# Kernel optimization log

Measured on AMD Instinct MI355X. Metric: run time of the kernel, lower is better.

## Reference

```python
import jax, jax.numpy as jnp
import numpy as np

Q, B, D, NH, DH, DI, M = 1024, 4, 1024, 16, 64, 4096, 1024
K = Q + M  # klen
SCALE_W = 0.02
LN_EPS = 1e-5


def _layer_norm(x, g, b):
    mu = jnp.mean(x, axis=-1, keepdims=True)
    var = jnp.var(x, axis=-1, keepdims=True)
    return (x - mu) * jax.lax.rsqrt(var + LN_EPS) * g + b


def _rel_shift(x):
    # x: [qlen, klen, bsz, n_head] -> Transformer-XL relative shift
    q, k = x.shape[0], x.shape[1]
    zero_pad = jnp.zeros((q, 1) + x.shape[2:], x.dtype)
    x_padded = jnp.concatenate([zero_pad, x], axis=1)          # [q, k+1, b, n]
    x_padded = x_padded.reshape((k + 1, q) + x.shape[2:])      # [k+1, q, b, n]
    return x_padded[1:].reshape(x.shape)


def setup_inputs() -> dict:
    key = jax.random.key(0)
    ks = jax.random.split(key, 12)
    f32 = jnp.float32
    inp = {
        "w": jax.random.normal(ks[0], (Q, B, D), f32),
        "r": jax.random.normal(ks[1], (K, 1, D), f32),
        "mems": jax.random.normal(ks[2], (M, B, D), f32),
        "qkv_w": SCALE_W * jax.random.normal(ks[3], (D, 3 * NH * DH), f32),
        "r_net_w": SCALE_W * jax.random.normal(ks[4], (D, NH * DH), f32),
        "o_w": SCALE_W * jax.random.normal(ks[5], (NH * DH, D), f32),
        "r_w_bias": SCALE_W * jax.random.normal(ks[6], (NH, DH), f32),
        "r_r_bias": SCALE_W * jax.random.normal(ks[7], (NH, DH), f32),
        "ln1_g": jnp.ones((D,), f32),
        "ln1_b": jnp.zeros((D,), f32),
        "ff_w1": SCALE_W * jax.random.normal(ks[8], (D, DI), f32),
        "ff_b1": jnp.zeros((DI,), f32),
        "ff_w2": SCALE_W * jax.random.normal(ks[9], (DI, D), f32),
        "ff_b2": jnp.zeros((D,), f32),
        "ln2_g": jnp.ones((D,), f32),
        "ln2_b": jnp.zeros((D,), f32),
        # causal mask with memory: query i attends to keys j <= i + mem_len
        "attn_mask": jnp.arange(K)[None, :] > (jnp.arange(Q)[:, None] + M),
    }
    return inp


def reference(w, r, mems, qkv_w, r_net_w, o_w, r_w_bias, r_r_bias,
              ln1_g, ln1_b, ff_w1, ff_b1, ff_w2, ff_b2, ln2_g, ln2_b,
              attn_mask):
    qlen, bsz = w.shape[0], w.shape[1]
    # --- relative multi-head attention (post-lnorm, mems concat) ---
    cat = jnp.concatenate([mems, w], axis=0)                   # [klen, b, d]
    w_heads = cat @ qkv_w                                      # [klen, b, 3*nh*dh]
    r_head_k = (r @ r_net_w).reshape(-1, NH, DH)               # [rlen, nh, dh]
    q_h, k_h, v_h = jnp.split(w_heads, 3, axis=-1)
    klen = k_h.shape[0]
    q_h = q_h[-qlen:].reshape(qlen, bsz, NH, DH)
    k_h = k_h.reshape(klen, bsz, NH, DH)
    v_h = v_h.reshape(klen, bsz, NH, DH)

    rw_q = q_h + r_w_bias[None, None]                          # [q, b, nh, dh]
    AC = jnp.einsum('ibnd,jbnd->ijbn', rw_q, k_h)
    rr_q = q_h + r_r_bias[None, None]
    BD = jnp.einsum('ibnd,jnd->ijbn', rr_q, r_head_k)
    BD = _rel_shift(BD)

    scale = 1.0 / (DH ** 0.5)
    attn_score = (AC + BD) * scale                             # [q, k, b, nh]
    attn_score = jnp.where(attn_mask[:, :, None, None], -jnp.inf, attn_score)
    attn_prob = jax.nn.softmax(attn_score, axis=1)
    attn_vec = jnp.einsum('ijbn,jbnd->ibnd', attn_prob, v_h)
    attn_out = attn_vec.reshape(qlen, bsz, NH * DH) @ o_w      # [q, b, d]
    out = _layer_norm(w + attn_out, ln1_g, ln1_b)

    # --- position-wise FFN (post-lnorm) ---
    core = jax.nn.relu(out @ ff_w1 + ff_b1) @ ff_w2 + ff_b2
    out = _layer_norm(out + core, ln2_g, ln2_b)
    return out
```

## Files before the change

### kernel.cpp

```cpp
#include <hip/hip_runtime.h>
#include <math.h>


#define QLEN 1024
#define BSZ  4
#define DMODEL 1024
#define NHEAD 16
#define DHEAD 64
#define DINNER 4096
#define MEMLEN 1024
#define KLEN 2048

typedef __attribute__((ext_vector_type(8))) short short8;
typedef __attribute__((ext_vector_type(4))) short short4_t;
typedef __attribute__((ext_vector_type(4))) float f32x4;

__device__ __forceinline__ unsigned short f2bf(float x) {
  union { float f; unsigned u; } cv; cv.f = x;
  const unsigned u = cv.u;
  return (unsigned short)((u + 0x7FFFu + ((u >> 16) & 1u)) >> 16);
}
__device__ __forceinline__ float bf2f(unsigned short b) {
  union { unsigned u; float f; } cv; cv.u = ((unsigned)b) << 16;
  return cv.f;
}

__device__ __forceinline__ void gload16(const void* g, void* l) {
  __builtin_amdgcn_global_load_lds(
      (const __attribute__((address_space(1))) unsigned int*)g,
      (__attribute__((address_space(3))) unsigned int*)l, 16, 0, 0);
}

__device__ __forceinline__ int chidx(int row, int kc) {
  return row * 4 + (kc ^ ((row >> 1) & 3));
}

template<int MODE>
__global__ __launch_bounds__(512) void mgemm2(
    const unsigned short* __restrict__ A, const unsigned short* __restrict__ Bt,
    unsigned short* __restrict__ Cb, const float* __restrict__ aux,
    unsigned short* __restrict__ oK, unsigned short* __restrict__ oV,
    int Kdim, int N)
{
  __shared__ __align__(16) char smem[98304];

  const int tid = threadIdx.x;
  const int lane = tid & 63, wv = tid >> 6;
  const int wr = wv >> 2, wc = wv & 3;
  const int quad = lane >> 4, l15 = lane & 15;

  const int gx = (int)gridDim.x;
  const int nwg = gx * (int)gridDim.y;
  const int flat = (int)blockIdx.y * gx + (int)blockIdx.x;
  const int swz = (flat & 7) * (nwg >> 3) + (flat >> 3);
  const int m0 = (swz / gx) * 256, n0 = (swz % gx) * 256;

  const int srow = tid >> 2;
  const int skc = (tid & 3) ^ ((srow >> 1) & 3);
  const unsigned short* pA0 = A + (size_t)(m0 + srow) * Kdim + skc * 8;
  const unsigned short* pA1 = A + (size_t)(m0 + 128 + srow) * Kdim + skc * 8;
  const unsigned short* pB0 = Bt + (size_t)(n0 + srow) * Kdim + skc * 8;
  const unsigned short* pB1 = Bt + (size_t)(n0 + 128 + srow) * Kdim + skc * 8;
  const int wb = (tid & 448) * 16;

  const int cch = (quad ^ ((l15 >> 1) & 3)) * 16;
  const int aoffb = wr * 8192 + l15 * 64 + cch;
  const int boffb = (wc >> 1) * 8192 + ((wc & 1) * 64 + l15) * 64 + cch;

  f32x4 acc[8][4] = {};

  const int nkt = Kdim >> 5;
  gload16(pA0, smem + wb);
  gload16(pA1, smem + 8192 + wb);
  gload16(pB0, smem + 49152 + wb);
  gload16(pB1, smem + 57344 + wb);
  pA0 += 32; pA1 += 32; pB0 += 32; pB1 += 32;
  gload16(pA0, smem + 16384 + wb);
  gload16(pA1, smem + 24576 + wb);
  gload16(pB0, smem + 65536 + wb);
  gload16(pB1, smem + 73728 + wb);
  pA0 += 32; pA1 += 32; pB0 += 32; pB1 += 32;

  int rbuf = 0;
  for (int kt = 0; kt < nkt; ++kt) {
    if (kt + 2 < nkt) {
      int wb3 = rbuf + 2; if (wb3 >= 3) wb3 -= 3;
      const int ab = wb3 * 16384, bb = 49152 + wb3 * 16384;
      gload16(pA0, smem + ab + wb);
      gload16(pA1, smem + ab + 8192 + wb);
      gload16(pB0, smem + bb + wb);
      gload16(pB1, smem + bb + 8192 + wb);
      pA0 += 32; pA1 += 32; pB0 += 32; pB1 += 32;
      asm volatile("s_waitcnt vmcnt(8)" ::: "memory");
    } else if (kt + 1 < nkt) {
      asm volatile("s_waitcnt vmcnt(4)" ::: "memory");
    } else {
      asm volatile("s_waitcnt vmcnt(0)" ::: "memory");
    }
    __builtin_amdgcn_s_barrier();

    const char* const abuf = smem + rbuf * 16384;
    const char* const bbuf = smem + 49152 + rbuf * 16384;

    short8 bfr[4], af[4];
#pragma unroll
    for (int j = 0; j < 4; ++j)
      bfr[j] = *(const short8*)(bbuf + boffb + j * 1024);
#pragma unroll
    for (int i = 0; i < 4; ++i)
      af[i] = *(const short8*)(abuf + aoffb + i * 1024);
    __builtin_amdgcn_s_setprio(1);
#pragma unroll
    for (int i = 0; i < 4; ++i)
#pragma unroll
      for (int j = 0; j < 4; ++j)
        acc[i][j] = __builtin_amdgcn_mfma_f32_16x16x32_bf16(
            af[i], bfr[j], acc[i][j], 0, 0, 0);
    __builtin_amdgcn_s_setprio(0);
    __builtin_amdgcn_s_barrier();

#pragma unroll
    for (int i = 0; i < 4; ++i)
      af[i] = *(const short8*)(abuf + aoffb + (i + 4) * 1024);
    __builtin_amdgcn_s_setprio(1);
#pragma unroll
    for (int i = 0; i < 4; ++i)
#pragma unroll
      for (int j = 0; j < 4; ++j)
        acc[i + 4][j] = __builtin_amdgcn_mfma_f32_16x16x32_bf16(
            af[i], bfr[j], acc[i + 4][j], 0, 0, 0);
    __builtin_amdgcn_s_setprio(0);
    asm volatile("s_waitcnt lgkmcnt(0)" ::: "memory");
    __builtin_amdgcn_s_barrier();
    rbuf += 1; if (rbuf == 3) rbuf = 0;
  }

  const int rb0 = m0 + wr * 128 + quad * 4;
  const int cb0 = n0 + wc * 64 + l15;
#pragma unroll
  for (int i = 0; i < 8; ++i) {
#pragma unroll
    for (int r = 0; r < 4; ++r) {
      const int grow = rb0 + i * 16 + r;
#pragma unroll
      for (int j = 0; j < 4; ++j) {
        const int gcol = cb0 + j * 16;
        const float v = acc[i][j][r];
        if constexpr (MODE == 0) {
          const int kkg = grow >> 2, b2 = grow & 3;
          const int sec = gcol >> 10, hn = (gcol >> 6) & 15, d = gcol & 63;
          const unsigned short bv = f2bf(v);
          if (sec == 0) {
            if (kkg >= MEMLEN)
              Cb[((size_t)(b2 * NHEAD + hn) * QLEN + (kkg - MEMLEN)) * DHEAD + d] = bv;
          } else if (sec == 1) {
            oK[((size_t)(b2 * NHEAD + hn) * KLEN + kkg) * DHEAD + d] = bv;
          } else {
            oV[((size_t)(b2 * NHEAD + hn) * KLEN + kkg) * DHEAD + d] = bv;
          }
        } else {
          Cb[(size_t)grow * N + gcol] = f2bf(fmaxf(v + aux[gcol], 0.f));
        }
      }
    }
  }
}

template<int MODE, int TN>
__global__ __launch_bounds__(256) void mgemm(
    const unsigned short* __restrict__ A, const unsigned short* __restrict__ Bt,
    float* __restrict__ C, unsigned short* __restrict__ Cb,
    const float* __restrict__ aux, const float* __restrict__ res,
    int Kdim, int N)
{
  constexpr int BUF = 8192 + TN * 64;
  __shared__ __align__(16) char smem[3 * BUF];

  const int tid = threadIdx.x;
  const int lane = tid & 63, wv = tid >> 6;

  const int gx = (int)gridDim.x;
  const int nwg = gx * (int)gridDim.y;
  const int flat = (int)blockIdx.y * gx + (int)blockIdx.x;
  const int swz = (flat & 7) * (nwg >> 3) + (flat >> 3);
  const int m0 = (swz / gx) * 128, n0 = (swz % gx) * TN;

  const unsigned short *gA0, *gA1, *gB0;
  {
    int c = tid, m = c >> 2, kc = (c & 3) ^ ((m >> 1) & 3);
    gA0 = A + (size_t)(m0 + m) * Kdim + kc * 8;
    c = 256 + tid; m = c >> 2; kc = (c & 3) ^ ((m >> 1) & 3);
    gA1 = A + (size_t)(m0 + m) * Kdim + kc * 8;
    c = tid; int nn = c >> 2; kc = (c & 3) ^ ((nn >> 1) & 3);
    gB0 = Bt + (size_t)(n0 + nn) * Kdim + kc * 8;
  }
  const int wvoff = (tid & 192) * 16;

  const int fr = lane & 15, kq = lane >> 4;
  constexpr int NJ = TN / 32;
  int aoff[4], boff[NJ];
#pragma unroll
  for (int t = 0; t < 4; ++t) {
    const int ra = (wv & 1) * 64 + t * 16 + fr;
    aoff[t] = chidx(ra, kq) * 16;
  }
#pragma unroll
  for (int t = 0; t < NJ; ++t) {
    const int rb = (wv >> 1) * (TN / 2) + t * 16 + fr;
    boff[t] = 8192 + chidx(rb, kq) * 16;
  }

  f32x4 acc[4][NJ] = {};

  {
    char* const b0 = smem + wvoff;
    gload16(gA0, b0);
    gload16(gA1, b0 + 4096);
    gload16(gB0, b0 + 8192);
    gA0 += 32; gA1 += 32; gB0 += 32;
    char* const b1 = smem + BUF + wvoff;
    gload16(gA0, b1);
    gload16(gA1, b1 + 4096);
    gload16(gB0, b1 + 8192);
    gA0 += 32; gA1 += 32; gB0 += 32;
  }

  int rbuf = 0;
  for (int k0 = 0; k0 < Kdim; k0 += 32) {
    if (k0 + 64 < Kdim) {
      int wb3 = rbuf + 2; if (wb3 >= 3) wb3 -= 3;
      char* const nb = smem + wb3 * BUF + wvoff;
      gload16(gA0, nb);
      gload16(gA1, nb + 4096);
      gload16(gB0, nb + 8192);
      gA0 += 32; gA1 += 32; gB0 += 32;
      asm volatile("s_waitcnt vmcnt(6)" ::: "memory");
    } else if (k0 + 32 < Kdim) {
      asm volatile("s_waitcnt vmcnt(3)" ::: "memory");
    } else {
      asm volatile("s_waitcnt vmcnt(0)" ::: "memory");
    }
    __builtin_amdgcn_s_barrier();

    const char* const cb = smem + rbuf * BUF;
    short8 af[4], bfr[NJ];
#pragma unroll
    for (int t = 0; t < 4; ++t) af[t] = *(const short8*)(cb + aoff[t]);
#pragma unroll
    for (int t = 0; t < NJ; ++t) bfr[t] = *(const short8*)(cb + boff[t]);
#pragma unroll
    for (int i = 0; i < 4; ++i)
#pragma unroll
      for (int j = 0; j < NJ; ++j)
        acc[i][j] = __builtin_amdgcn_mfma_f32_16x16x32_bf16(
            af[i], bfr[j], acc[i][j], 0, 0, 0);

    asm volatile("s_waitcnt lgkmcnt(0)" ::: "memory");
    __builtin_amdgcn_s_barrier();
    rbuf += 1; if (rbuf == 3) rbuf = 0;
  }

  const int rbase = m0 + (wv & 1) * 64 + (lane >> 4) * 4;
  const int cbase = n0 + (wv >> 1) * (TN / 2) + (lane & 15);
#pragma unroll
  for (int i = 0; i < 4; ++i) {
#pragma unroll
    for (int r = 0; r < 4; ++r) {
      const int grow = rbase + i * 16 + r;
#pragma unroll
      for (int j = 0; j < NJ; ++j) {
        const int gcol = cbase + j * 16;
        const float v = acc[i][j][r];
        if constexpr (MODE == 1) {
          const int hn = gcol >> 6, d = gcol & 63;
          Cb[((size_t)hn * KLEN + grow) * DHEAD + d] = f2bf(v);
        } else if constexpr (MODE == 2) {
          C[(size_t)grow * N + gcol] = v + res[(size_t)grow * N + gcol];
        } else {
          C[(size_t)grow * N + gcol] = v + aux[gcol] + res[(size_t)grow * N + gcol];
        }
      }
    }
  }
}

__global__ __launch_bounds__(256) void transpose_v(
    const unsigned short* __restrict__ Vh, unsigned short* __restrict__ Vt)
{
  __shared__ unsigned short t[64 * 80];
  const int j0 = (int)blockIdx.x * 64;
  const int bn = (int)blockIdx.y;
  const int tid = threadIdx.x;
#pragma unroll
  for (int it = 0; it < 2; ++it) {
    const int f = it * 256 + tid;
    const int j = f >> 3, d8 = (f & 7) * 8;
    const short8 v = *(const short8*)(Vh + ((size_t)bn * KLEN + j0 + j) * DHEAD + d8);
    *(short8*)(t + j * 80 + d8) = v;
  }
  __syncthreads();
  const int d = tid >> 2, jseg = (tid & 3) * 16;
  short8 o0, o1;
#pragma unroll
  for (int e = 0; e < 8; ++e) o0[e] = (short)t[(jseg + e) * 80 + d];
#pragma unroll
  for (int e = 0; e < 8; ++e) o1[e] = (short)t[(jseg + 8 + e) * 80 + d];
  unsigned short* op = Vt + ((size_t)bn * DHEAD + d) * KLEN + j0 + jseg;
  *(short8*)op = o0;
  *(short8*)(op + 8) = o1;
}

__global__ __launch_bounds__(256) void cast_all(
    const float* __restrict__ mems, const float* __restrict__ w,
    const float* __restrict__ r, unsigned short* __restrict__ Xcat,
    unsigned short* __restrict__ Rb16)
{
  const size_t i = ((size_t)blockIdx.x * 256 + threadIdx.x) * 8;
  const float* src;
  unsigned short* dst;
  if (i < 4194304)       { src = mems + i;          dst = Xcat + i; }
  else if (i < 8388608)  { src = w + (i - 4194304); dst = Xcat + i; }
  else                   { src = r + (i - 8388608); dst = Rb16 + (i - 8388608); }
  const float4 x = *(const float4*)src;
  const float4 y = *(const float4*)(src + 4);
  short8 v;
  v[0] = (short)f2bf(x.x); v[1] = (short)f2bf(x.y);
  v[2] = (short)f2bf(x.z); v[3] = (short)f2bf(x.w);
  v[4] = (short)f2bf(y.x); v[5] = (short)f2bf(y.y);
  v[6] = (short)f2bf(y.z); v[7] = (short)f2bf(y.w);
  *(short8*)dst = v;
}

__global__ __launch_bounds__(256) void transpose_all(
    const float* __restrict__ qkv_w, const float* __restrict__ r_net_w,
    const float* __restrict__ o_w, const float* __restrict__ ff_w1,
    const float* __restrict__ ff_w2,
    unsigned short* __restrict__ Wqkv, unsigned short* __restrict__ Wr,
    unsigned short* __restrict__ Wo, unsigned short* __restrict__ W1,
    unsigned short* __restrict__ W2)
{
  const int bid = (int)blockIdx.x;
  const float* in; unsigned short* out; int R, C, xt, loc;
  if (bid < 768)        { in = qkv_w;   out = Wqkv; R = 1024; C = 3072; xt = 48; loc = bid; }
  else if (bid < 1024)  { in = r_net_w; out = Wr;   R = 1024; C = 1024; xt = 16; loc = bid - 768; }
  else if (bid < 1280)  { in = o_w;     out = Wo;   R = 1024; C = 1024; xt = 16; loc = bid - 1024; }
  else if (bid < 2304)  { in = ff_w1;   out = W1;   R = 1024; C = 4096; xt = 64; loc = bid - 1280; }
  else                  { in = ff_w2;   out = W2;   R = 4096; C = 1024; xt = 16; loc = bid - 2304; }
  const int c0 = (loc % xt) * 64, r0 = (loc / xt) * 64;

  __shared__ float t[64][65];
  const int tid = threadIdx.x;
  const int rr = tid >> 4, cc = (tid & 15) * 4;
#pragma unroll
  for (int it = 0; it < 4; ++it) {
    const int rw = rr + it * 16;
    const float4 v = *(const float4*)(in + (size_t)(r0 + rw) * C + c0 + cc);
    t[rw][cc] = v.x; t[rw][cc + 1] = v.y; t[rw][cc + 2] = v.z; t[rw][cc + 3] = v.w;
  }
  __syncthreads();
  const int oc = tid >> 2, ob = (tid & 3) * 16;
#pragma unroll
  for (int j4 = 0; j4 < 4; ++j4) {
    short4_t o;
#pragma unroll
    for (int j = 0; j < 4; ++j) o[j] = (short)f2bf(t[ob + j4 * 4 + j][oc]);
    *(short4_t*)(out + (size_t)(c0 + oc) * R + r0 + ob + j4 * 4) = o;
  }
}

__global__ __launch_bounds__(256, 2) void attn_mfma(
    const unsigned short* __restrict__ Qh, const unsigned short* __restrict__ Kh,
    const unsigned short* __restrict__ Vt, const unsigned short* __restrict__ Rk,
    const float* __restrict__ rwb, const float* __restrict__ rrb,
    float* __restrict__ Opart0, float* __restrict__ Opart1,
    float* __restrict__ den0, float* __restrict__ den1)
{
  __shared__ __align__(16) char smem[65536];

  const int tid = threadIdx.x;
  const int lane = tid & 63, wv = tid >> 6;
  const int quad = lane >> 4, l15 = lane & 15;

  const int bid0 = (int)blockIdx.y * 32 + (int)blockIdx.x;
  const int slot = bid0 >> 3;
  const int bn = (bid0 & 7) * 8 + (slot >> 5);
  const int inner = slot & 31;
  const int it = inner >> 1, sp = inner & 1;
  const int i0 = it * 64;
  const int n = bn & 15;

  const int nch = 17 + it;
  const int h = (nch + 1) >> 1;
  const int lo = sp ? h : 0, hi = sp ? nch : h;

  const unsigned short* __restrict__ Qb = Qh + (size_t)bn * QLEN * DHEAD;
  const unsigned short* __restrict__ Kb = Kh + (size_t)bn * KLEN * DHEAD;
  const unsigned short* __restrict__ Vb = Vt + (size_t)bn * DHEAD * KLEN;
  const unsigned short* __restrict__ Rb = Rk + (size_t)n * KLEN * DHEAD;

  short8 qk[2], qr[2];
  {
    const int qrow = i0 + wv * 16 + l15;
    const unsigned short* qp = Qb + (size_t)qrow * DHEAD + quad * 8;
    const float* wp = rwb + n * DHEAD + quad * 8;
    const float* rp = rrb + n * DHEAD + quad * 8;
#pragma unroll
    for (int ks = 0; ks < 2; ++ks) {
      const short8 q8 = *(const short8*)(qp + ks * 32);
#pragma unroll
      for (int e = 0; e < 8; ++e) {
        const float qv = bf2f((unsigned short)q8[e]);
        qk[ks][e] = (short)f2bf(qv + wp[ks * 32 + e]);
        qr[ks][e] = (short)f2bf(qv + rp[ks * 32 + e]);
      }
    }
  }

  int srcl[4];
  bool condE[4];
#pragma unroll
  for (int r = 0; r < 4; ++r) {
    const int E = l15 - quad * 4 - r + 15;
    srcl[r] = (lane & 48) | (E & 15);
    condE[r] = (E >= 16);
  }

  f32x4 O[4] = {};
  float rden[4] = {0.f, 0.f, 0.f, 0.f};
  const int wvoff = (tid & 192) * 16;

  {
    const int j0 = lo * 64;
    const int g64 = lo - it + 15;
    const int rb3 = (g64 % 3) * 64;
#pragma unroll
    for (int t2 = 0; t2 < 2; ++t2) {
      const int s = t2 * 256 + tid;
      const int row = s >> 3, kc = (s & 7) ^ (row & 7);
      gload16(Kb + (((size_t)(j0 + row)) << 6) + kc * 8,
              smem + t2 * 4096 + wvoff);
    }
#pragma unroll
    for (int t2 = 0; t2 < 2; ++t2) {
      const int s = t2 * 256 + tid;
      const int row = s >> 3, kc = (s & 7) ^ (row & 7);
      gload16(Vb + (((size_t)row) << 11) + j0 + kc * 8,
              smem + 16384 + t2 * 4096 + wvoff);
    }
    const int gw = j0 - i0 + 960;
#pragma unroll
    for (int t2 = 0; t2 < 4; ++t2) {
      const int rr = t2 * 32 + (tid >> 3);
      const int gr = gw + rr;
      const int kc = (tid & 7) ^ (rr & 7);
      int pb = rb3 + t2 * 32; if (pb >= 192) pb -= 192;
      gload16(Rb + (((size_t)gr) << 6) + kc * 8,
              smem + 32768 + pb * 128 + wvoff);
    }
  }

  int cur = 0;
  for (int ch = lo; ch < hi; ++ch) {
    const int j0 = ch * 64;
    const int g64 = ch - it + 15;
    const int rb3 = (g64 % 3) * 64;
    const int gw = j0 - i0 + 960;

    asm volatile("s_waitcnt lgkmcnt(0)" ::: "memory");
    __builtin_amdgcn_s_barrier();

    if (ch + 1 < hi) {
      const int nb = cur ^ 1;
      const int j0n = j0 + 64;
#pragma unroll
      for (int t2 = 0; t2 < 2; ++t2) {
        const int s = t2 * 256 + tid;
        const int row = s >> 3, kc = (s & 7) ^ (row & 7);
        gload16(Kb + (((size_t)(j0n + row)) << 6) + kc * 8,
                smem + nb * 8192 + t2 * 4096 + wvoff);
      }
#pragma unroll
      for (int t2 = 0; t2 < 2; ++t2) {
        const int s = t2 * 256 + tid;
        const int row = s >> 3, kc = (s & 7) ^ (row & 7);
        gload16(Vb + (((size_t)row) << 11) + j0n + kc * 8,
                smem + 16384 + nb * 8192 + t2 * 4096 + wvoff);
      }
#pragma unroll
      for (int t2 = 0; t2 < 2; ++t2) {
        const int rr = t2 * 32 + (tid >> 3);
        const int gr = gw + 128 + rr;
        const int kc = (tid & 7) ^ (rr & 7);
        int pb = rb3 + 128 + t2 * 32; if (pb >= 192) pb -= 192;
        gload16(Rb + (((size_t)gr) << 6) + kc * 8,
                smem + 32768 + pb * 128 + wvoff);
      }
      asm volatile("s_waitcnt vmcnt(6)" ::: "memory");
    } else {
      asm volatile("s_waitcnt vmcnt(0)" ::: "memory");
    }
    __builtin_amdgcn_s_barrier();

    const char* const kbase = smem + cur * 8192;
    const char* const vbase = smem + 16384 + cur * 8192;

    f32x4 sk[4];
#pragma unroll
    for (int jt = 0; jt < 4; ++jt) {
      f32x4 a = {0.f, 0.f, 0.f, 0.f};
#pragma unroll
      for (int ks = 0; ks < 2; ++ks) {
        const int frr = jt * 16 + l15;
        const int c = (ks * 4 + quad) ^ (l15 & 7);
        const short8 kf = *(const short8*)(kbase + (frr * 8 + c) * 16);
        a = __builtin_amdgcn_mfma_f32_16x16x32_bf16(qk[ks], kf, a, 0, 0, 0);
      }
      sk[jt] = a;
    }
    f32x4 uu[5];
#pragma unroll
    for (int s = 0; s < 5; ++s) {
      f32x4 a = {0.f, 0.f, 0.f, 0.f};
      int frr = rb3 + (3 - wv + s) * 16 + l15;
      if (frr >= 192) frr -= 192;
#pragma unroll
      for (int ks = 0; ks < 2; ++ks) {
        const int c = (ks * 4 + quad) ^ (l15 & 7);
        const short8 rf = *(const short8*)(smem + 32768 + (frr * 8 + c) * 16);
        a = __builtin_amdgcn_mfma_f32_16x16x32_bf16(qr[ks], rf, a, 0, 0, 0);
      }
      uu[s] = a;
    }

    float rot[5][4];
#pragma unroll
    for (int s = 0; s < 5; ++s)
#pragma unroll
      for (int r = 0; r < 4; ++r)
        rot[s][r] = __shfl(uu[s][r], srcl[r], 64);

    unsigned short* const Ps = (unsigned short*)(smem + 57344);
#pragma unroll
    for (int jt = 0; jt < 4; ++jt) {
      const int jl = jt * 16 + l15;
#pragma unroll
      for (int r = 0; r < 4; ++r) {
        const int il = wv * 16 + quad * 4 + r;
        const int dj = (j0 + jl) - (i0 + il);
        const float uv = condE[r] ? rot[jt + 1][r] : rot[jt][r];
        const float sv = (sk[jt][r] + uv) * 0.125f;
        const float p = (dj <= 1024) ? __expf(sv) : 0.f;
        rden[r] += p;
        Ps[(il * 8 + ((jl >> 3) ^ (il & 7))) * 8 + (jl & 7)] = f2bf(p);
      }
    }

#pragma unroll
    for (int ks = 0; ks < 2; ++ks) {
      const int frp = wv * 16 + l15;
      const int cp = (ks * 4 + quad) ^ (l15 & 7);
      const short8 pf = *(const short8*)(smem + 57344 + (frp * 8 + cp) * 16);
#pragma unroll
      for (int dt = 0; dt < 4; ++dt) {
        const int vr = dt * 16 + l15;
        const short8 vf = *(const short8*)(vbase + (vr * 8 + cp) * 16);
        O[dt] = __builtin_amdgcn_mfma_f32_16x16x32_bf16(pf, vf, O[dt], 0, 0, 0);
      }
    }
    cur ^= 1;
  }

#pragma unroll
  for (int m = 1; m < 16; m <<= 1)
#pragma unroll
    for (int r = 0; r < 4; ++r)
      rden[r] += __shfl_xor(rden[r], m, 64);

  float* const Op = sp ? Opart1 : Opart0;
  float* const dp = sp ? den1 : den0;
  const size_t ob = (size_t)(bn * 16 + it) * 64;
#pragma unroll
  for (int r = 0; r < 4; ++r) {
    const int il = wv * 16 + quad * 4 + r;
#pragma unroll
    for (int dt = 0; dt < 4; ++dt)
      Op[(ob + il) * 64 + dt * 16 + l15] = O[dt][r];
    if (l15 == 0) dp[ob + il] = rden[r];
  }
}

__global__ __launch_bounds__(256) void attn_combine(
    const float* __restrict__ O0, const float* __restrict__ O1,
    const float* __restrict__ d0, const float* __restrict__ d1,
    unsigned short* __restrict__ AVb)
{
  const int blk = (int)blockIdx.x;
  const int bn = blk >> 4, it = blk & 15;
  const int b = bn >> 4, n = bn & 15;
  const int tid = threadIdx.x;
  const int il = tid >> 2, ds = (tid & 3) * 16;
  const size_t base = ((size_t)blk * 64 + il) * 64 + ds;
  const float inv = 1.f / (d0[blk * 64 + il] + d1[blk * 64 + il]);
  short8 o0, o1;
#pragma unroll
  for (int g = 0; g < 2; ++g) {
    const float4 a = *(const float4*)(O0 + base + g * 8);
    const float4 bb = *(const float4*)(O1 + base + g * 8);
    const float4 a2 = *(const float4*)(O0 + base + g * 8 + 4);
    const float4 b2 = *(const float4*)(O1 + base + g * 8 + 4);
    short8& o = g ? o1 : o0;
    o[0] = (short)f2bf((a.x + bb.x) * inv);  o[1] = (short)f2bf((a.y + bb.y) * inv);
    o[2] = (short)f2bf((a.z + bb.z) * inv);  o[3] = (short)f2bf((a.w + bb.w) * inv);
    o[4] = (short)f2bf((a2.x + b2.x) * inv); o[5] = (short)f2bf((a2.y + b2.y) * inv);
    o[6] = (short)f2bf((a2.z + b2.z) * inv); o[7] = (short)f2bf((a2.w + b2.w) * inv);
  }
  unsigned short* op =
      AVb + ((size_t)(it * 64 + il) * BSZ + b) * DMODEL + n * DHEAD + ds;
  *(short8*)op = o0;
  *(short8*)(op + 8) = o1;
}

__global__ __launch_bounds__(256) void ln_kernel(
    float* __restrict__ X, const float* __restrict__ gw,
    const float* __restrict__ bw, unsigned short* __restrict__ bfo)
{
  const int row = blockIdx.x, tid = threadIdx.x;
  float* rp = X + (size_t)row * DMODEL;
  const float4 x = *(const float4*)(rp + tid * 4);
  float s = x.x + x.y + x.z + x.w;
  float q = x.x * x.x + x.y * x.y + x.z * x.z + x.w * x.w;
#pragma unroll
  for (int m = 1; m < 64; m <<= 1) {
    s += __shfl_xor(s, m, 64);
    q += __shfl_xor(q, m, 64);
  }
  __shared__ float ss[4], sq[4];
  if ((tid & 63) == 0) { ss[tid >> 6] = s; sq[tid >> 6] = q; }
  __syncthreads();
  s = ss[0] + ss[1] + ss[2] + ss[3];
  q = sq[0] + sq[1] + sq[2] + sq[3];
  const float mu = s * (1.f / DMODEL);
  const float var = q * (1.f / DMODEL) - mu * mu;
  const float rstd = rsqrtf(var + 1e-5f);
  const float4 g4 = *(const float4*)(gw + tid * 4);
  const float4 b4 = *(const float4*)(bw + tid * 4);
  float4 y;
  y.x = (x.x - mu) * rstd * g4.x + b4.x;
  y.y = (x.y - mu) * rstd * g4.y + b4.y;
  y.z = (x.z - mu) * rstd * g4.z + b4.z;
  y.w = (x.w - mu) * rstd * g4.w + b4.w;
  *(float4*)(rp + tid * 4) = y;
  if (bfo) {
    short4_t o;
    o[0] = (short)f2bf(y.x); o[1] = (short)f2bf(y.y);
    o[2] = (short)f2bf(y.z); o[3] = (short)f2bf(y.w);
    *(short4_t*)(bfo + (size_t)row * DMODEL + tid * 4) = o;
  }
}

extern "C" void kernel_launch(void* const* d_in, const int* in_sizes, int n_in,
                              void* d_out, int out_size, void* d_ws,
                              size_t ws_size, hipStream_t stream)
{
  const float* w       = (const float*)d_in[0];
  const float* r       = (const float*)d_in[1];
  const float* mems    = (const float*)d_in[2];
  const float* qkv_w   = (const float*)d_in[3];
  const float* r_net_w = (const float*)d_in[4];
  const float* o_w     = (const float*)d_in[5];
  const float* r_w_bias= (const float*)d_in[6];
  const float* r_r_bias= (const float*)d_in[7];
  const float* ln1_g   = (const float*)d_in[8];
  const float* ln1_b   = (const float*)d_in[9];
  const float* ff_w1   = (const float*)d_in[10];
  const float* ff_b1   = (const float*)d_in[11];
  const float* ff_w2   = (const float*)d_in[12];
  const float* ff_b2   = (const float*)d_in[13];
  const float* ln2_g   = (const float*)d_in[14];
  const float* ln2_b   = (const float*)d_in[15];
  float* out = (float*)d_out;

  float* X1 = (float*)d_ws;
  unsigned short* Qh   = (unsigned short*)(X1 + 4194304);
  unsigned short* Kh   = Qh + 4194304;
  unsigned short* Vt   = Kh + 8388608;
  unsigned short* Rk   = Vt + 8388608;
  unsigned short* Xcat = Rk + 2097152 + 8192;
  unsigned short* Wqkv = Xcat + 8388608;
  unsigned short* Wr   = Wqkv + 3145728;
  unsigned short* Wo   = Wr + 1048576;
  unsigned short* W1   = Wo + 1048576;
  unsigned short* W2   = W1 + 4194304;
  float* den0 = (float*)(W2 + 4194304);
  float* den1 = den0 + 65536;
  unsigned short* AVb  = (unsigned short*)(den1 + 65536);
  unsigned short* Vh     = (unsigned short*)X1;
  unsigned short* Rb16   = AVb;
  float* Opart0          = (float*)X1;
  float* Opart1          = (float*)Xcat;
  unsigned short* X1b    = Qh;
  unsigned short* H      = Kh;

  const dim3 blk(256);
  const dim3 blk2(512);

  cast_all<<<dim3(5120), blk, 0, stream>>>(mems, w, r, Xcat, Rb16);
  transpose_all<<<dim3(3328), blk, 0, stream>>>(
      qkv_w, r_net_w, o_w, ff_w1, ff_w2, Wqkv, Wr, Wo, W1, W2);

  mgemm2<0><<<dim3(12, 32), blk2, 0, stream>>>(
      Xcat, Wqkv, Qh, nullptr, Kh, Vh, DMODEL, 3 * DMODEL);
  transpose_v<<<dim3(32, 64), blk, 0, stream>>>(Vh, Vt);
  mgemm<1, 64><<<dim3(16, 16), blk, 0, stream>>>(
      Rb16, Wr, nullptr, Rk, nullptr, nullptr, DMODEL, DMODEL);
  attn_mfma<<<dim3(32, 64), blk, 0, stream>>>(
      Qh, Kh, Vt, Rk, r_w_bias, r_r_bias, Opart0, Opart1, den0, den1);
  attn_combine<<<dim3(1024), blk, 0, stream>>>(Opart0, Opart1, den0, den1, AVb);
  mgemm<2, 64><<<dim3(16, 32), blk, 0, stream>>>(
      AVb, Wo, X1, nullptr, nullptr, w, DMODEL, DMODEL);
  ln_kernel<<<dim3(4096), blk, 0, stream>>>(X1, ln1_g, ln1_b, X1b);
  mgemm2<3><<<dim3(16, 16), blk2, 0, stream>>>(
      X1b, W1, H, ff_b1, nullptr, nullptr, DMODEL, DINNER);
  mgemm<4, 64><<<dim3(16, 32), blk, 0, stream>>>(
      H, W2, out, nullptr, ff_b2, X1, DINNER, DMODEL);
  ln_kernel<<<dim3(4096), blk, 0, stream>>>(out, ln2_g, ln2_b, nullptr);

  (void)in_sizes; (void)n_in; (void)out_size; (void)ws_size;
}
```

Baseline: 521.2 us.

## Load R fragments directly from global to shrink LDS and raise occupancy

The attention kernel no longer stages the relative-position R tile in a rotating shared-memory ring buffer. Each wave now loads its R fragments straight from global memory into registers every chunk. This cuts shared memory from 64KB to 40KB, and the launch bound is raised to allow 3 blocks per CU. The cost is uncoalesced, unprefetched global loads on the critical path each iteration, plus more register pressure under a tighter register budget.

```diff
diff --git a/kernel.cpp b/kernel.cpp
--- a/kernel.cpp
+++ b/kernel.cpp
@@ -368,14 +368,14 @@
   }
 }
 
-__global__ __launch_bounds__(256, 2) void attn_mfma(
+__global__ __launch_bounds__(256, 3) void attn_mfma(
     const unsigned short* __restrict__ Qh, const unsigned short* __restrict__ Kh,
     const unsigned short* __restrict__ Vt, const unsigned short* __restrict__ Rk,
     const float* __restrict__ rwb, const float* __restrict__ rrb,
     float* __restrict__ Opart0, float* __restrict__ Opart1,
     float* __restrict__ den0, float* __restrict__ den1)
 {
-  __shared__ __align__(16) char smem[65536];
+  __shared__ __align__(16) char smem[40960];
 
   const int tid = threadIdx.x;
   const int lane = tid & 63, wv = tid >> 6;
@@ -431,8 +431,6 @@
 
   {
     const int j0 = lo * 64;
-    const int g64 = lo - it + 15;
-    const int rb3 = (g64 % 3) * 64;
 #pragma unroll
     for (int t2 = 0; t2 < 2; ++t2) {
       const int s = t2 * 256 + tid;
@@ -447,23 +445,11 @@
       gload16(Vb + (((size_t)row) << 11) + j0 + kc * 8,
               smem + 16384 + t2 * 4096 + wvoff);
     }
-    const int gw = j0 - i0 + 960;
-#pragma unroll
-    for (int t2 = 0; t2 < 4; ++t2) {
-      const int rr = t2 * 32 + (tid >> 3);
-      const int gr = gw + rr;
-      const int kc = (tid & 7) ^ (rr & 7);
-      int pb = rb3 + t2 * 32; if (pb >= 192) pb -= 192;
-      gload16(Rb + (((size_t)gr) << 6) + kc * 8,
-              smem + 32768 + pb * 128 + wvoff);
-    }
   }
 
   int cur = 0;
   for (int ch = lo; ch < hi; ++ch) {
     const int j0 = ch * 64;
-    const int g64 = ch - it + 15;
-    const int rb3 = (g64 % 3) * 64;
     const int gw = j0 - i0 + 960;
 
     asm volatile("s_waitcnt lgkmcnt(0)" ::: "memory");
@@ -486,20 +472,20 @@
         gload16(Vb + (((size_t)row) << 11) + j0n + kc * 8,
                 smem + 16384 + nb * 8192 + t2 * 4096 + wvoff);
       }
-#pragma unroll
-      for (int t2 = 0; t2 < 2; ++t2) {
-        const int rr = t2 * 32 + (tid >> 3);
-        const int gr = gw + 128 + rr;
-        const int kc = (tid & 7) ^ (rr & 7);
-        int pb = rb3 + 128 + t2 * 32; if (pb >= 192) pb -= 192;
-        gload16(Rb + (((size_t)gr) << 6) + kc * 8,
-                smem + 32768 + pb * 128 + wvoff);
-      }
-      asm volatile("s_waitcnt vmcnt(6)" ::: "memory");
+      asm volatile("s_waitcnt vmcnt(4)" ::: "memory");
     } else {
       asm volatile("s_waitcnt vmcnt(0)" ::: "memory");
     }
     __builtin_amdgcn_s_barrier();
+
+    short8 rfr0[5], rfr1[5];
+#pragma unroll
+    for (int s = 0; s < 5; ++s) {
+      const int gr = gw + (3 - wv + s) * 16 + l15;
+      const unsigned short* rp = Rb + (((size_t)gr) << 6) + quad * 8;
+      rfr0[s] = *(const short8*)rp;
+      rfr1[s] = *(const short8*)(rp + 32);
+    }
 
     const char* const kbase = smem + cur * 8192;
     const char* const vbase = smem + 16384 + cur * 8192;
@@ -521,14 +507,8 @@
 #pragma unroll
     for (int s = 0; s < 5; ++s) {
       f32x4 a = {0.f, 0.f, 0.f, 0.f};
-      int frr = rb3 + (3 - wv + s) * 16 + l15;
-      if (frr >= 192) frr -= 192;
-#pragma unroll
-      for (int ks = 0; ks < 2; ++ks) {
-        const int c = (ks * 4 + quad) ^ (l15 & 7);
-        const short8 rf = *(const short8*)(smem + 32768 + (frr * 8 + c) * 16);
-        a = __builtin_amdgcn_mfma_f32_16x16x32_bf16(qr[ks], rf, a, 0, 0, 0);
-      }
+      a = __builtin_amdgcn_mfma_f32_16x16x32_bf16(qr[0], rfr0[s], a, 0, 0, 0);
+      a = __builtin_amdgcn_mfma_f32_16x16x32_bf16(qr[1], rfr1[s], a, 0, 0, 0);
       uu[s] = a;
     }
 
@@ -539,7 +519,7 @@
       for (int r = 0; r < 4; ++r)
         rot[s][r] = __shfl(uu[s][r], srcl[r], 64);
 
-    unsigned short* const Ps = (unsigned short*)(smem + 57344);
+    unsigned short* const Ps = (unsigned short*)(smem + 32768);
 #pragma unroll
     for (int jt = 0; jt < 4; ++jt) {
       const int jl = jt * 16 + l15;
@@ -559,7 +539,7 @@
     for (int ks = 0; ks < 2; ++ks) {
       const int frp = wv * 16 + l15;
       const int cp = (ks * 4 + quad) ^ (l15 & 7);
-      const short8 pf = *(const short8*)(smem + 57344 + (frp * 8 + cp) * 16);
+      const short8 pf = *(const short8*)(smem + 32768 + (frp * 8 + cp) * 16);
 #pragma unroll
       for (int dt = 0; dt < 4; ++dt) {
         const int vr = dt * 16 + l15;
```

Measured after the change: 555.2 us. 6.5% more time.
